# Performance work log

Hardware: AMD Instinct MI355X
Metric: run time of the kernel (lower is better)

The kernel has to match this reference:

```python
import jax, jax.numpy as jnp
import numpy as np

NUM_GROUP = 512   # G: number of FPS centers
GROUP_SIZE = 32   # k: KNN neighborhood size
B, N = 16, 8192


def _fps_indices(pts, n):
    """Farthest point sampling on pts [N,3] -> n int32 indices (first index = 0, matching CUDA FPS)."""
    Np = pts.shape[0]

    def body(carry, _):
        dists, last = carry
        d = jnp.sum((pts - pts[last]) ** 2, axis=-1)
        dists = jnp.minimum(dists, d)
        nxt = jnp.argmax(dists).astype(jnp.int32)
        return (dists, nxt), nxt

    init = (jnp.full((Np,), jnp.inf, dtype=pts.dtype), jnp.int32(0))
    _, rest = jax.lax.scan(body, init, None, length=n - 1)
    return jnp.concatenate([jnp.zeros((1,), jnp.int32), rest])


def _pairwise_sqdist(centers, pts):
    """centers [G,3], pts [N,3] -> [G,N] squared distances via the GEMM form (avoids [G,N,3])."""
    c2 = jnp.sum(centers * centers, axis=-1)[:, None]   # [G,1]
    p2 = jnp.sum(pts * pts, axis=-1)[None, :]           # [1,N]
    cp = jnp.einsum('gd,nd->gn', centers, pts)          # [G,N]
    return c2 + p2 - 2.0 * cp


def setup_inputs() -> dict:
    key = jax.random.key(0)
    k1, k2, k3 = jax.random.split(key, 3)
    xyz = jax.random.normal(k1, (B, N, 3), dtype=jnp.float32)
    gt_points = jax.random.normal(k2, (B, N, 3), dtype=jnp.float32)
    labels = jax.random.randint(k3, (B, N), 0, 50, dtype=jnp.int32)
    return {"xyz": xyz, "gt_points": gt_points, "labels": labels}


def reference(xyz, gt_points, labels):
    # FPS centers (indices are shared for xyz and gt_points, as in fps())
    fidx = jax.vmap(lambda p: _fps_indices(p, NUM_GROUP))(xyz)                  # [B,G] int32
    center = jnp.take_along_axis(xyz, fidx[:, :, None], axis=1)                 # [B,G,3]
    gt_center = jnp.take_along_axis(gt_points, fidx[:, :, None], axis=1)        # [B,G,3]

    # KNN: for each center, k nearest points in xyz (ascending distance)
    d2 = jax.vmap(_pairwise_sqdist)(center, xyz)                                # [B,G,N]
    _, idx = jax.lax.top_k(-d2, GROUP_SIZE)                                     # [B,G,k]

    # Gather + per-group centering (the fusible gather/subtract the module does)
    neighborhood = jax.vmap(lambda x, i: x[i])(xyz, idx)                        # [B,G,k,3]
    neighborhood = neighborhood - center[:, :, None, :]
    gt_neighborhood = jax.vmap(lambda x, i: x[i])(gt_points, idx)               # [B,G,k,3]
    gt_neighborhood = gt_neighborhood - gt_center[:, :, None, :]
    grp_labels = jax.vmap(lambda l, i: l[i])(labels, idx)[..., None]            # [B,G,k,1]

    return neighborhood, center, gt_neighborhood, grp_labels
```

## Files before the change

### kernel.cpp

```cpp
#include <hip/hip_runtime.h>
#include <math.h>

#define NPTS 8192
#define NB   16
#define NG   512
#define KNN  32

typedef float v2f __attribute__((ext_vector_type(2)));

__device__ __forceinline__ v2f pk_add(v2f a, v2f b) {
    v2f r; asm("v_pk_add_f32 %0, %1, %2" : "=v"(r) : "v"(a), "v"(b)); return r;
}
__device__ __forceinline__ v2f pk_mul(v2f a, v2f b) {
    v2f r; asm("v_pk_mul_f32 %0, %1, %2" : "=v"(r) : "v"(a), "v"(b)); return r;
}
__device__ __forceinline__ v2f pk_fma(v2f a, v2f b, v2f c) {
    v2f r; asm("v_pk_fma_f32 %0, %1, %2, %3" : "=v"(r) : "v"(a), "v"(b), "v"(c)); return r;
}

#define DPP_MAXF(v, ctrl)                                                       \
    v = fmaxf(v, __int_as_float(__builtin_amdgcn_update_dpp(                    \
            0, __float_as_int(v), (ctrl), 0xF, 0xF, true)))
#define DPP_MINU(v, ctrl)                                                       \
    {   unsigned _o = (unsigned)__builtin_amdgcn_update_dpp(                    \
            (int)0x7FFFFFFF, (int)(v), (ctrl), 0xF, 0xF, false);                \
        v = (v < _o) ? v : _o; }

__global__ __launch_bounds__(256) void fps_kernel(const float* __restrict__ xyz,
                                                  int* __restrict__ fidx)
{
#pragma clang fp contract(off)
    __shared__ float s_xyz[NPTS * 3];
    __shared__ unsigned long long skey[2][4];

    const int b    = blockIdx.x;
    const int t    = threadIdx.x;
    const int w    = t >> 6;
    const int lane = t & 63;
    const float* base = xyz + (size_t)b * NPTS * 3;

    for (int j = t; j < NPTS * 3 / 4; j += 256)
        ((float4*)s_xyz)[j] = ((const float4*)base)[j];
    __syncthreads();

    float px[32], py[32], pz[32], dd[32];
#pragma unroll
    for (int j = 0; j < 32; ++j) {
        int p = t + (j << 8);
        px[j] = s_xyz[3*p+0];
        py[j] = s_xyz[3*p+1];
        pz[j] = s_xyz[3*p+2];
        dd[j] = INFINITY;
    }
    if (t == 0) fidx[b*NG] = 0;

    float cx = s_xyz[0], cy = s_xyz[1], cz = s_xyz[2];

    for (int it = 1; it < NG; ++it) {
        const int s = it & 1;
        float bv = -INFINITY; int sl = 0;
#pragma unroll
        for (int j = 0; j < 32; ++j) {
            float dx = px[j]-cx, dy = py[j]-cy, dz = pz[j]-cz;
            float d  = (dx*dx + dy*dy) + dz*dz;
            float nd = fminf(dd[j], d);
            dd[j] = nd;
            if (nd > bv) { bv = nd; sl = j; }
        }
        const int bi = t + (sl << 8);

        float mv = bv;
        DPP_MAXF(mv, 0x111);
        DPP_MAXF(mv, 0x112);
        DPP_MAXF(mv, 0x114);
        DPP_MAXF(mv, 0x118);
        DPP_MAXF(mv, 0x142);
        DPP_MAXF(mv, 0x143);
        const unsigned Mbits = (unsigned)__builtin_amdgcn_readlane(__float_as_int(mv), 63);

        unsigned long long mask = __ballot(__float_as_uint(bv) == Mbits);
        unsigned wIdx;
        if (__popcll(mask) == 1) {
            wIdx = (unsigned)__builtin_amdgcn_readlane(bi, (int)__ffsll(mask) - 1);
        } else {
            unsigned cand = (__float_as_uint(bv) == Mbits) ? (unsigned)bi : 0x7FFFFFFFu;
            DPP_MINU(cand, 0x111);
            DPP_MINU(cand, 0x112);
            DPP_MINU(cand, 0x114);
            DPP_MINU(cand, 0x118);
            DPP_MINU(cand, 0x142);
            DPP_MINU(cand, 0x143);
            wIdx = (unsigned)__builtin_amdgcn_readlane((int)cand, 63);
        }

        if (lane == 0)
            skey[s][w] = ((unsigned long long)Mbits << 32) | (unsigned)(8191 - wIdx);
        __syncthreads();
        unsigned long long km = skey[s][0];
        km = (skey[s][1] > km) ? skey[s][1] : km;
        km = (skey[s][2] > km) ? skey[s][2] : km;
        km = (skey[s][3] > km) ? skey[s][3] : km;
        const int ix = 8191 - (int)(km & 0xFFFFu);
        cx = s_xyz[3*ix+0]; cy = s_xyz[3*ix+1]; cz = s_xyz[3*ix+2];
        if (t == 0) fidx[b*NG + it] = ix;
    }
}

__global__ __launch_bounds__(1024) void knn_kernel(const float* __restrict__ xyz,
                                                   const float* __restrict__ gtp,
                                                   const int* __restrict__ labels,
                                                   const int* __restrict__ fidx,
                                                   float* __restrict__ out)
{
#pragma clang fp contract(off)
    __shared__ float spx[NPTS], spy[NPTS], spz[NPTS];
    __shared__ float sdl[16][64];
    __shared__ int   sil[16][64];

    const int tb   = threadIdx.x;
    const int lane = tb & 63;
    const int w    = tb >> 6;
    const int gid  = (blockIdx.x << 4) + w;
    const int b    = gid >> 9;

    const float* base  = xyz + (size_t)b * NPTS * 3;
    const float* gbase = gtp + (size_t)b * NPTS * 3;

    for (int j = tb; j < NPTS * 3 / 4; j += 1024) {
        float4 v = ((const float4*)base)[j];
        int f0 = 4*j;
#pragma unroll
        for (int e = 0; e < 4; ++e) {
            int f = f0 + e;
            float val = (e==0) ? v.x : (e==1) ? v.y : (e==2) ? v.z : v.w;
            int p = f / 3;
            int c = f - 3*p;
            float* dst = (c==0) ? spx : (c==1) ? spy : spz;
            dst[p] = val;
        }
    }
    __syncthreads();

    const int   cidx = fidx[gid];
    const float cx = spx[cidx], cy = spy[cidx], cz = spz[cidx];
    const float c2 = (cx*cx + cy*cy) + cz*cz;
    const v2f cx2 = (v2f){cx,cx}, cy2 = (v2f){cy,cy}, cz2 = (v2f){cz,cz};
    const v2f c22 = (v2f){c2,c2}, mm2 = (v2f){-2.0f,-2.0f};
    const unsigned long long lmask = (lane == 63) ? ~0ull >> 1 : (1ull << lane) - 1ull;

    float m = INFINITY;
#pragma unroll 4
    for (int i = 0; i < 64; ++i) {
        int q = 2*lane + (i << 7);
        v2f xv = *(const v2f*)&spx[q];
        v2f yv = *(const v2f*)&spy[q];
        v2f zv = *(const v2f*)&spz[q];
        v2f p2 = pk_add(pk_add(pk_mul(xv,xv), pk_mul(yv,yv)), pk_mul(zv,zv));
        v2f cp = pk_fma(cz2, zv, pk_fma(cy2, yv, pk_mul(cx2, xv)));
        v2f dv = pk_add(pk_add(c22, p2), pk_mul(cp, mm2));
        m = fminf(m, dv.x);
        m = fminf(m, dv.y);
    }

    {
        float v = m;
#pragma unroll
        for (int k = 2; k <= 64; k <<= 1) {
#pragma unroll
            for (int j = k >> 1; j >= 1; j >>= 1) {
                float o = __shfl_xor(v, j);
                bool keep_min = (((lane & j) == 0) != ((lane & k) != 0));
                v = keep_min ? fminf(v, o) : fmaxf(v, o);
            }
        }
        m = __shfl(v, 31);
    }
    const float T_ub = m;

    int cnt = 0;
    for (int i = 0; i < 64; ++i) {
        int q = 2*lane + (i << 7);
        v2f xv = *(const v2f*)&spx[q];
        v2f yv = *(const v2f*)&spy[q];
        v2f zv = *(const v2f*)&spz[q];
        v2f p2 = pk_add(pk_add(pk_mul(xv,xv), pk_mul(yv,yv)), pk_mul(zv,zv));
        v2f cp = pk_fma(cz2, zv, pk_fma(cy2, yv, pk_mul(cx2, xv)));
        v2f dv = pk_add(pk_add(c22, p2), pk_mul(cp, mm2));
        bool t0 = (dv.x <= T_ub);
        unsigned long long m0 = __ballot(t0);
        if (t0) {
            int slot = cnt + __popcll(m0 & lmask);
            if (slot < 64) { sdl[w][slot] = dv.x; sil[w][slot] = q; }
        }
        cnt += __popcll(m0);
        bool t1 = (dv.y <= T_ub);
        unsigned long long m1 = __ballot(t1);
        if (t1) {
            int slot = cnt + __popcll(m1 & lmask);
            if (slot < 64) { sdl[w][slot] = dv.y; sil[w][slot] = q + 1; }
        }
        cnt += __popcll(m1);
    }

    int myIdx = 0;
    if (cnt <= 64) {
        float d  = (lane < cnt) ? sdl[w][lane] : INFINITY;
        int   ix = (lane < cnt) ? sil[w][lane] : 0x7fffffff;
#pragma unroll
        for (int k = 2; k <= 64; k <<= 1) {
#pragma unroll
            for (int j = k >> 1; j >= 1; j >>= 1) {
                float od = __shfl_xor(d, j);
                int   oi = __shfl_xor(ix, j);
                bool keep_min = (((lane & j) == 0) != ((lane & k) != 0));
                bool o_less   = (od < d) || (od == d && oi < ix);
                bool take_o   = keep_min ? o_less : !o_less;
                if (take_o) { d = od; ix = oi; }
            }
        }
        myIdx = ix;
    } else {
        float ld[KNN]; int li[KNN];
#pragma unroll
        for (int j = 0; j < KNN; ++j) { ld[j] = INFINITY; li[j] = 0x7fffffff; }
        for (int i = 0; i < NPTS/64; ++i) {
            int p = lane + (i << 6);
            float x = spx[p], y = spy[p], z = spz[p];
            float p2 = (x*x + y*y) + z*z;
            float cp = fmaf(cz, z, fmaf(cy, y, cx*x));
            float d  = (c2 + p2) - 2.0f*cp;
            if (d < ld[KNN-1]) {
                float cv = d; int ci = p;
#pragma unroll
                for (int j = 0; j < KNN; ++j) {
                    if (cv < ld[j]) {
                        float tv = ld[j]; int ti = li[j];
                        ld[j] = cv; li[j] = ci;
                        cv = tv; ci = ti;
                    }
                }
            }
        }
#pragma unroll
        for (int r = 0; r < KNN; ++r) {
            float bv = ld[0]; int bi = li[0]; int bl = lane;
#pragma unroll
            for (int off = 32; off >= 1; off >>= 1) {
                float ov = __shfl_xor(bv, off);
                int   oi = __shfl_xor(bi, off);
                int   ol = __shfl_xor(bl, off);
                if (ov < bv || (ov == bv && oi < bi)) { bv = ov; bi = oi; bl = ol; }
            }
            if (lane == r) myIdx = bi;
            if (lane == bl) {
#pragma unroll
                for (int j = 0; j < KNN-1; ++j) { ld[j] = ld[j+1]; li[j] = li[j+1]; }
                ld[KNN-1] = INFINITY; li[KNN-1] = 0x7fffffff;
            }
        }
    }

    float* out_nb  = out;
    float* out_c   = out + 786432;
    float* out_gnb = out + 811008;
    float* out_lb  = out + 1597440;

    const float gcx = gbase[3*cidx+0], gcy = gbase[3*cidx+1], gcz = gbase[3*cidx+2];

    if (lane < KNN) {
        int p = myIdx;
        size_t o3 = ((size_t)gid * KNN + lane) * 3;
        out_nb[o3+0]  = spx[p] - cx;
        out_nb[o3+1]  = spy[p] - cy;
        out_nb[o3+2]  = spz[p] - cz;
        out_gnb[o3+0] = gbase[3*p+0] - gcx;
        out_gnb[o3+1] = gbase[3*p+1] - gcy;
        out_gnb[o3+2] = gbase[3*p+2] - gcz;
        out_lb[(size_t)gid*KNN + lane] = (float)labels[(size_t)b*NPTS + p];
    }
    if (lane == 0) {
        out_c[gid*3+0] = cx; out_c[gid*3+1] = cy; out_c[gid*3+2] = cz;
    }
}

extern "C" void kernel_launch(void* const* d_in, const int* in_sizes, int n_in,
                              void* d_out, int out_size, void* d_ws, size_t ws_size,
                              hipStream_t stream)
{
    const float* xyz    = (const float*)d_in[0];
    const float* gtp    = (const float*)d_in[1];
    const int*   labels = (const int*)d_in[2];
    int*   fidx = (int*)d_ws;
    float* outp = (float*)d_out;

    hipLaunchKernelGGL(fps_kernel, dim3(NB), dim3(256), 0, stream, xyz, fidx);
    hipLaunchKernelGGL(knn_kernel, dim3(NB*NG/16), dim3(1024), 0, stream,
                       xyz, gtp, labels, fidx, outp);
}
```

Before: 558.1 us.

## Restructure FPS argmax into max-tree, ballot index search, and shared coords

The per-thread running argmax in the FPS loop is split into a plain min-update followed by a max3 reduction tree, so the update loop carries no compare-select dependency chain. The winning index is then recovered from per-slot wave ballots against the wave maximum instead of a DPP min-reduction over candidate indices. Each wave's lane 0 also writes its winner's coordinates to shared memory, so after the barrier every thread picks the next center with vectorized LDS reads and selects, with no dependent s_xyz lookup. This trades 32 ballots per iteration for a shorter critical path in the serial 511-iteration loop, and the lowest slot-then-lane tie-break gives the same lowest-index choice as before.

```diff
diff --git a/kernel.cpp b/kernel.cpp
--- a/kernel.cpp
+++ b/kernel.cpp
@@ -21,10 +21,10 @@
 #define DPP_MAXF(v, ctrl)                                                       \
     v = fmaxf(v, __int_as_float(__builtin_amdgcn_update_dpp(                    \
             0, __float_as_int(v), (ctrl), 0xF, 0xF, true)))
-#define DPP_MINU(v, ctrl)                                                       \
-    {   unsigned _o = (unsigned)__builtin_amdgcn_update_dpp(                    \
-            (int)0x7FFFFFFF, (int)(v), (ctrl), 0xF, 0xF, false);                \
-        v = (v < _o) ? v : _o; }
+
+__device__ __forceinline__ float max3f(float a, float b, float c) {
+    return fmaxf(fmaxf(a, b), c);
+}
 
 __global__ __launch_bounds__(256) void fps_kernel(const float* __restrict__ xyz,
                                                   int* __restrict__ fidx)
@@ -32,6 +32,7 @@
 #pragma clang fp contract(off)
     __shared__ float s_xyz[NPTS * 3];
     __shared__ unsigned long long skey[2][4];
+    __shared__ __align__(16) float scoord[2][12];
 
     const int b    = blockIdx.x;
     const int t    = threadIdx.x;
@@ -58,16 +59,30 @@
 
     for (int it = 1; it < NG; ++it) {
         const int s = it & 1;
-        float bv = -INFINITY; int sl = 0;
+
 #pragma unroll
         for (int j = 0; j < 32; ++j) {
             float dx = px[j]-cx, dy = py[j]-cy, dz = pz[j]-cz;
             float d  = (dx*dx + dy*dy) + dz*dz;
-            float nd = fminf(dd[j], d);
-            dd[j] = nd;
-            if (nd > bv) { bv = nd; sl = j; }
-        }
-        const int bi = t + (sl << 8);
+            dd[j] = fminf(dd[j], d);
+        }
+
+        float r0 = max3f(dd[0],  dd[1],  dd[2]);
+        float r1 = max3f(dd[3],  dd[4],  dd[5]);
+        float r2 = max3f(dd[6],  dd[7],  dd[8]);
+        float r3 = max3f(dd[9],  dd[10], dd[11]);
+        float r4 = max3f(dd[12], dd[13], dd[14]);
+        float r5 = max3f(dd[15], dd[16], dd[17]);
+        float r6 = max3f(dd[18], dd[19], dd[20]);
+        float r7 = max3f(dd[21], dd[22], dd[23]);
+        float r8 = max3f(dd[24], dd[25], dd[26]);
+        float r9 = max3f(dd[27], dd[28], dd[29]);
+        float ra = fmaxf(dd[30], dd[31]);
+        float s0 = max3f(r0, r1, r2);
+        float s1 = max3f(r3, r4, r5);
+        float s2 = max3f(r6, r7, r8);
+        float s3 = fmaxf(r9, ra);
+        float bv = fmaxf(max3f(s0, s1, s2), s3);
 
         float mv = bv;
         DPP_MAXF(mv, 0x111);
@@ -78,31 +93,49 @@
         DPP_MAXF(mv, 0x143);
         const unsigned Mbits = (unsigned)__builtin_amdgcn_readlane(__float_as_int(mv), 63);
 
-        unsigned long long mask = __ballot(__float_as_uint(bv) == Mbits);
-        unsigned wIdx;
-        if (__popcll(mask) == 1) {
-            wIdx = (unsigned)__builtin_amdgcn_readlane(bi, (int)__ffsll(mask) - 1);
-        } else {
-            unsigned cand = (__float_as_uint(bv) == Mbits) ? (unsigned)bi : 0x7FFFFFFFu;
-            DPP_MINU(cand, 0x111);
-            DPP_MINU(cand, 0x112);
-            DPP_MINU(cand, 0x114);
-            DPP_MINU(cand, 0x118);
-            DPP_MINU(cand, 0x142);
-            DPP_MINU(cand, 0x143);
-            wIdx = (unsigned)__builtin_amdgcn_readlane((int)cand, 63);
-        }
-
-        if (lane == 0)
+        unsigned long long acc = 0ull; int jw = 0;
+#pragma unroll
+        for (int j = 0; j < 32; ++j) {
+            unsigned long long mj = __ballot(__float_as_uint(dd[j]) == Mbits);
+            bool take = (acc == 0ull) & (mj != 0ull);
+            acc = take ? mj : acc;
+            jw  = take ? j : jw;
+        }
+        const unsigned wIdx = ((unsigned)jw << 8) | ((unsigned)w << 6)
+                            | (unsigned)(__ffsll((unsigned long long)acc) - 1);
+
+        if (lane == 0) {
+            float wx = s_xyz[3*wIdx+0];
+            float wy = s_xyz[3*wIdx+1];
+            float wz = s_xyz[3*wIdx+2];
             skey[s][w] = ((unsigned long long)Mbits << 32) | (unsigned)(8191 - wIdx);
+            scoord[s][w*3+0] = wx;
+            scoord[s][w*3+1] = wy;
+            scoord[s][w*3+2] = wz;
+        }
         __syncthreads();
-        unsigned long long km = skey[s][0];
-        km = (skey[s][1] > km) ? skey[s][1] : km;
-        km = (skey[s][2] > km) ? skey[s][2] : km;
-        km = (skey[s][3] > km) ? skey[s][3] : km;
-        const int ix = 8191 - (int)(km & 0xFFFFu);
-        cx = s_xyz[3*ix+0]; cy = s_xyz[3*ix+1]; cz = s_xyz[3*ix+2];
-        if (t == 0) fidx[b*NG + it] = ix;
+
+        ulonglong2 k01 = *(const ulonglong2*)&skey[s][0];
+        ulonglong2 k23 = *(const ulonglong2*)&skey[s][2];
+        float4 q0 = *(const float4*)&scoord[s][0];
+        float4 q1 = *(const float4*)&scoord[s][4];
+        float4 q2 = *(const float4*)&scoord[s][8];
+        bool s01 = (k01.y > k01.x);
+        unsigned long long kA = s01 ? k01.y : k01.x;
+        float ax = s01 ? q0.w : q0.x;
+        float ay = s01 ? q1.x : q0.y;
+        float az = s01 ? q1.y : q0.z;
+        bool s23 = (k23.y > k23.x);
+        unsigned long long kB = s23 ? k23.y : k23.x;
+        float bx = s23 ? q2.y : q1.z;
+        float by = s23 ? q2.z : q1.w;
+        float bz = s23 ? q2.w : q2.x;
+        bool sF = (kB > kA);
+        unsigned long long km = sF ? kB : kA;
+        cx = sF ? bx : ax;
+        cy = sF ? by : ay;
+        cz = sF ? bz : az;
+        if (t == 0) fidx[b*NG + it] = 8191 - (int)(km & 0xFFFFu);
     }
 }
 
```

After: 851.9 us. +52.6%, slower.
